# Optimization experiments

Measured on AMD Instinct MI355X. Metric: run time of the kernel, lower is better.

## Reference

```python
import jax, jax.numpy as jnp
import numpy as np

N, D, K, P = 4096, 256, 16, 3
MAXDEG = K + 1          # self loop guarantees deg >= 1, randint caps deg <= K+1
TAU, LAM, BETA, MARGIN = 0.8, 0.5, 1.0, 0.1
EPS_PD = 1e-6           # F.pairwise_distance eps (added to the difference)


def _make_adj(k):
    nbr = jax.random.randint(k, (N, K), 0, N)
    m = jnp.zeros((N, N), jnp.float32)
    m = m.at[jnp.arange(N)[:, None], nbr].set(1.0)
    m = m.at[jnp.arange(N), jnp.arange(N)].set(1.0)
    return m / m.sum(1, keepdims=True)  # row-normalized metapath adjacency


def setup_inputs():
    key = jax.random.key(0)
    ks = jax.random.split(key, 12)
    g = 1.414 * (2.0 / (D + D)) ** 0.5  # xavier_normal gain=1.414
    return {
        "h": jax.random.normal(ks[0], (N, D), jnp.float32),
        "mps": jnp.stack([_make_adj(ks[1 + i]) for i in range(P)]),
        "W_gcn": jax.random.normal(ks[4], (P, D, D), jnp.float32) * g,
        "b_gcn": jnp.zeros((P, D), jnp.float32),
        "prelu_a": jnp.full((P,), 0.25, jnp.float32),
        "att_fc_W": jax.random.normal(ks[5], (D, D), jnp.float32) * g,
        "att_fc_b": jnp.zeros((D,), jnp.float32),
        "att_vec": jax.random.normal(ks[6], (D,), jnp.float32) * g,
        "proj_W1": jax.random.normal(ks[7], (D, D), jnp.float32) * g,
        "proj_b1": jnp.zeros((D,), jnp.float32),
        "proj_W2": jax.random.normal(ks[8], (D, D), jnp.float32) * g,
        "proj_b2": jnp.zeros((D,), jnp.float32),
    }


def _gcn(h, adj, W, b, a):
    out = adj @ (h @ W.T) + b          # spmm(adj, fc(h)) + bias
    return jnp.where(out > 0, out, a * out)  # PReLU


def _node_loss(emb, adj):
    # vectorized form of the per-node nonzero/pairwise_distance loop
    mask = adj > 0                      # [N, N]
    deg = mask.sum(1)                   # [N], >= 1 via self loops
    # stable argsort: neighbors first (ascending index), matching torch.nonzero order
    pos_idx = jnp.argsort(~mask, axis=1)[:, :MAXDEG]
    neg_idx = jnp.argsort(mask, axis=1)[:, :MAXDEG]   # first deg non-neighbors
    anc = emb[:, None, :]               # anchor expanded over pairs
    dp = jnp.sum((anc - emb[pos_idx] + EPS_PD) ** 2, -1)  # [N, MAXDEG]
    dn = jnp.sum((anc - emb[neg_idx] + EPS_PD) ** 2, -1)
    valid = jnp.arange(MAXDEG)[None, :] < deg[:, None]
    per = jnp.maximum(dp - dn + MARGIN, 0.0) * valid
    return jnp.sum(per.sum(1) / deg.astype(emb.dtype))  # per-node mean, summed


def _proj(z, W1, b1, W2, b2):
    return jax.nn.elu(z @ W1.T + b1) @ W2.T + b2


def _contrast(z1, z2, pos, W1, b1, W2, b2):
    p1 = _proj(z1, W1, b1, W2, b2)
    p2 = _proj(z2, W1, b1, W2, b2)
    n1 = jnp.linalg.norm(p1, axis=-1, keepdims=True)
    n2 = jnp.linalg.norm(p2, axis=-1, keepdims=True)
    sim = jnp.exp((p1 @ p2.T) / (n1 * n2.T) / TAU)     # [N, N]
    m12 = sim / (sim.sum(1, keepdims=True) + 1e-8)
    m21 = sim.T / (sim.T.sum(1, keepdims=True) + 1e-8)
    l12 = -jnp.log((m12 * pos).sum(-1)).mean()
    l21 = -jnp.log((m21 * pos).sum(-1)).mean()
    return LAM * l12 + (1.0 - LAM) * l21


def reference(h, mps, W_gcn, b_gcn, prelu_a, att_fc_W, att_fc_b, att_vec,
              proj_W1, proj_b1, proj_W2, proj_b2):
    embeds = [_gcn(h, mps[i], W_gcn[i], b_gcn[i], prelu_a[i]) for i in range(P)]
    node_loss = sum(_node_loss(embeds[i], mps[i]) for i in range(P))
    # faithful to original control flow: i==0 inner loop overwrites self.loss,
    # so only the (0, P-1) pair survives from i==0
    closs = _contrast(embeds[0], embeds[P - 1], mps[0], proj_W1, proj_b1, proj_W2, proj_b2)
    for i in range(1, P - 1):
        for j in range(i + 1, P):
            closs = closs + _contrast(embeds[i], embeds[j], mps[i], proj_W1, proj_b1, proj_W2, proj_b2)
    # semantic attention over metapaths
    sp = jnp.stack([jnp.tanh(e @ att_fc_W.T + att_fc_b).mean(0) for e in embeds])  # [P, D]
    beta = jax.nn.softmax(sp @ att_vec)                                            # [P]
    z_mp = jnp.einsum('p,pnd->nd', beta, jnp.stack(embeds))
    return z_mp, node_loss + BETA * closs
```

## Files before the change

kernel.cpp:

```cpp
#include <hip/hip_runtime.h>
#include <hip/hip_bf16.h>

constexpr int N = 4096;
constexpr int D = 256;
constexpr int P = 3;
constexpr int MAXDEG = 17;
constexpr float TAU = 0.8f;
constexpr float MARGIN = 0.1f;
constexpr float EPS_PD = 1e-6f;

constexpr int LDP = 40;

constexpr int OFF_H    = 0;
constexpr int OFF_WG   = 1048576;
constexpr int OFF_ATTW = 1245184;
constexpr int OFF_W1   = 1310720;
constexpr int OFF_W2   = 1376256;
constexpr int OFF_BG   = 1441792;
constexpr int OFF_ATTB = 1442560;
constexpr int OFF_AV   = 1442816;
constexpr int OFF_PA   = 1443072;
constexpr int OFF_B1   = 1443328;
constexpr int OFF_B2   = 1443584;
constexpr int CONV_TOTAL = 1443840;

typedef __attribute__((ext_vector_type(8))) short bfrag8;
typedef __attribute__((ext_vector_type(4))) float facc4;

__device__ inline facc4 mfma16(bfrag8 a, bfrag8 b, facc4 c) {
    return __builtin_amdgcn_mfma_f32_16x16x32_bf16(a, b, c, 0, 0, 0);
}
__device__ inline float b2f(__hip_bfloat16 v) { return __bfloat162float(v); }
__device__ inline float bfbits2f(unsigned short u) {
    return __uint_as_float(((unsigned int)u) << 16);
}
__device__ inline unsigned short f2bfbits(float v) {
    __hip_bfloat16 t = __float2bfloat16(v);
    return *(unsigned short*)&t;
}
__device__ inline int get_bf(const int* __restrict__ counter) { return counter[0] > 100; }

__device__ inline float load_in(const void* p, size_t i, int bf) {
    return bf ? __bfloat162float(((const __hip_bfloat16*)p)[i])
              : ((const float*)p)[i];
}

__device__ __forceinline__ void gl_lds16(const __hip_bfloat16* g, __hip_bfloat16* l) {
    __builtin_amdgcn_global_load_lds(
        (const __attribute__((address_space(1))) unsigned int*)g,
        (__attribute__((address_space(3))) unsigned int*)l, 16, 0, 0);
}

__global__ void detect_dtype(const unsigned int* __restrict__ w, int nwords,
                             int* __restrict__ counter) {
    int stride = gridDim.x * blockDim.x;
    int c = 0;
    for (int i = blockIdx.x * blockDim.x + threadIdx.x; i < nwords; i += stride) {
        unsigned int x = w[i];
        if ((x & 0xFFFF0000u) == 0u && x != 0u) c++;
    }
    for (int s = 32; s > 0; s >>= 1) c += __shfl_down(c, s);
    if ((threadIdx.x & 63) == 0 && c > 0) atomicAdd(counter, c);
}

__global__ void convert_all(const void* h, const void* wg, const void* attw,
                            const void* w1, const void* w2, const void* bg,
                            const void* attb, const void* av, const void* pa,
                            const void* b1, const void* b2,
                            const int* __restrict__ counter,
                            __hip_bfloat16* __restrict__ dst) {
    int bf = get_bf(counter);
    const void* srcs[11] = {h, wg, attw, w1, w2, bg, attb, av, pa, b1, b2};
    const int offs[11] = {OFF_H, OFF_WG, OFF_ATTW, OFF_W1, OFF_W2, OFF_BG,
                          OFF_ATTB, OFF_AV, OFF_PA, OFF_B1, OFF_B2};
    const int lens[11] = {1048576, 196608, 65536, 65536, 65536, 768, 256, 256, 3, 256, 256};
    int stride = gridDim.x * blockDim.x;
    int t0 = blockIdx.x * blockDim.x + threadIdx.x;
    #pragma unroll
    for (int s = 0; s < 11; s++) {
        for (int i = t0; i < lens[s]; i += stride)
            dst[offs[s] + i] = __float2bfloat16(load_in(srcs[s], i, bf));
    }
}

__global__ void extract_sparse(const void* __restrict__ mps, const int* __restrict__ counter,
                               int* __restrict__ nbr_idx, float* __restrict__ nbr_val,
                               int* __restrict__ neg_idx, int* __restrict__ deg) {
    int bf = get_bf(counter);
    int row = blockIdx.x;
    int t = threadIdx.x;
    __shared__ int cnt;
    __shared__ int sidx[32];
    __shared__ float sval[32];
    if (t == 0) cnt = 0;
    __syncthreads();
    int e0 = t * 16;
    if (bf) {
        const uint4* base = (const uint4*)((const __hip_bfloat16*)mps + (size_t)row * N + e0);
        #pragma unroll
        for (int v = 0; v < 2; v++) {
            uint4 w = base[v];
            unsigned int ws[4] = {w.x, w.y, w.z, w.w};
            #pragma unroll
            for (int j = 0; j < 4; j++) {
                unsigned short lo = (unsigned short)(ws[j] & 0xFFFFu);
                unsigned short hi = (unsigned short)(ws[j] >> 16);
                if (lo) { int k = atomicAdd(&cnt, 1); if (k < 32) { sidx[k] = e0 + v * 8 + j * 2;     sval[k] = bfbits2f(lo); } }
                if (hi) { int k = atomicAdd(&cnt, 1); if (k < 32) { sidx[k] = e0 + v * 8 + j * 2 + 1; sval[k] = bfbits2f(hi); } }
            }
        }
    } else {
        const float4* base = (const float4*)((const float*)mps + (size_t)row * N + e0);
        #pragma unroll
        for (int v = 0; v < 4; v++) {
            float4 w = base[v];
            float ws[4] = {w.x, w.y, w.z, w.w};
            #pragma unroll
            for (int j = 0; j < 4; j++)
                if (ws[j] > 0.f) { int k = atomicAdd(&cnt, 1); if (k < 32) { sidx[k] = e0 + v * 4 + j; sval[k] = ws[j]; } }
        }
    }
    __syncthreads();
    if (t == 0) {
        int dg = cnt; if (dg > MAXDEG) dg = MAXDEG;
        for (int i = 1; i < dg; i++) {
            int ki = sidx[i]; float kv = sval[i]; int j = i - 1;
            while (j >= 0 && sidx[j] > ki) { sidx[j+1] = sidx[j]; sval[j+1] = sval[j]; j--; }
            sidx[j+1] = ki; sval[j+1] = kv;
        }
        deg[row] = dg;
        int* oi = nbr_idx + (size_t)row * MAXDEG;
        float* ov = nbr_val + (size_t)row * MAXDEG;
        int* ng = neg_idx + (size_t)row * MAXDEG;
        for (int i = 0; i < MAXDEG; i++) { oi[i] = (i < dg) ? sidx[i] : 0; ov[i] = (i < dg) ? sval[i] : 0.f; }
        int c = 0, j = 0, found = 0;
        while (found < MAXDEG) {
            if (j < dg && sidx[j] == c) { j++; c++; continue; }
            ng[found++] = c++;
        }
    }
}

template <int ACT>
__global__ void gemm_mfma(const __hip_bfloat16* __restrict__ Abase, size_t strideA,
                          const __hip_bfloat16* __restrict__ Bbase, size_t strideB,
                          const __hip_bfloat16* __restrict__ bias, size_t strideBias,
                          __hip_bfloat16* __restrict__ Cbase, size_t strideC) {
    int z = blockIdx.z;
    const __hip_bfloat16* A = Abase + (size_t)z * strideA;
    const __hip_bfloat16* B = Bbase + (size_t)z * strideB;
    __shared__ __align__(16) __hip_bfloat16 As[64 * LDP];
    __shared__ __align__(16) __hip_bfloat16 Bs[64 * LDP];
    int bm = blockIdx.x * 64, bn = blockIdx.y * 64;
    int tid = threadIdx.x, wave = tid >> 6, lane = tid & 63;
    int quad = lane >> 4, l15 = lane & 15;
    int wr = (wave & 1) * 32, wc = (wave >> 1) * 32;
    facc4 acc[2][2] = {};
    int sr = tid >> 2, kq = (tid & 3) * 8;
    for (int k0 = 0; k0 < D; k0 += 32) {
        *(bfrag8*)&As[sr * LDP + kq] = *(const bfrag8*)&A[(size_t)(bm + sr) * D + k0 + kq];
        *(bfrag8*)&Bs[sr * LDP + kq] = *(const bfrag8*)&B[(size_t)(bn + sr) * D + k0 + kq];
        __syncthreads();
        bfrag8 af[2], bfr[2];
        #pragma unroll
        for (int mi = 0; mi < 2; mi++)
            af[mi] = *(const bfrag8*)&As[(wr + mi * 16 + l15) * LDP + quad * 8];
        #pragma unroll
        for (int ni = 0; ni < 2; ni++)
            bfr[ni] = *(const bfrag8*)&Bs[(wc + ni * 16 + l15) * LDP + quad * 8];
        #pragma unroll
        for (int mi = 0; mi < 2; mi++)
            #pragma unroll
            for (int ni = 0; ni < 2; ni++)
                acc[mi][ni] = mfma16(af[mi], bfr[ni], acc[mi][ni]);
        __syncthreads();
    }
    #pragma unroll
    for (int mi = 0; mi < 2; mi++) {
        #pragma unroll
        for (int ni = 0; ni < 2; ni++) {
            int col = bn + wc + ni * 16 + l15;
            #pragma unroll
            for (int r = 0; r < 4; r++) {
                int row = bm + wr + mi * 16 + quad * 4 + r;
                float v = acc[mi][ni][r];
                if (bias) v += b2f(bias[col]);
                if (ACT == 1) v = v > 0.f ? v : expm1f(v);
                Cbase[(size_t)z * strideC + (size_t)row * D + col] = __float2bfloat16(v);
            }
        }
    }
}

__global__ void gemm_dual(const __hip_bfloat16* __restrict__ embBase,
                          const __hip_bfloat16* __restrict__ conv,
                          __hip_bfloat16* __restrict__ xbuf,
                          float* __restrict__ spacc) {
    int z = blockIdx.z;
    const __hip_bfloat16* A = embBase + (size_t)z * N * D;
    const __hip_bfloat16* Ba = conv + OFF_ATTW;
    const __hip_bfloat16* Bw = conv + OFF_W1;
    __shared__ __align__(16) __hip_bfloat16 As[64 * LDP];
    __shared__ __align__(16) __hip_bfloat16 Bsa[64 * LDP];
    __shared__ __align__(16) __hip_bfloat16 Bsw[64 * LDP];
    int bm = blockIdx.x * 64, bn = blockIdx.y * 64;
    int tid = threadIdx.x, wave = tid >> 6, lane = tid & 63;
    int quad = lane >> 4, l15 = lane & 15;
    int wr = (wave & 1) * 32, wc = (wave >> 1) * 32;
    facc4 accA[2][2] = {};
    facc4 accW[2][2] = {};
    int sr = tid >> 2, kq = (tid & 3) * 8;
    for (int k0 = 0; k0 < D; k0 += 32) {
        *(bfrag8*)&As[sr * LDP + kq]  = *(const bfrag8*)&A[(size_t)(bm + sr) * D + k0 + kq];
        *(bfrag8*)&Bsa[sr * LDP + kq] = *(const bfrag8*)&Ba[(size_t)(bn + sr) * D + k0 + kq];
        *(bfrag8*)&Bsw[sr * LDP + kq] = *(const bfrag8*)&Bw[(size_t)(bn + sr) * D + k0 + kq];
        __syncthreads();
        bfrag8 af[2], ba[2], bw[2];
        #pragma unroll
        for (int mi = 0; mi < 2; mi++)
            af[mi] = *(const bfrag8*)&As[(wr + mi * 16 + l15) * LDP + quad * 8];
        #pragma unroll
        for (int ni = 0; ni < 2; ni++) {
            ba[ni] = *(const bfrag8*)&Bsa[(wc + ni * 16 + l15) * LDP + quad * 8];
            bw[ni] = *(const bfrag8*)&Bsw[(wc + ni * 16 + l15) * LDP + quad * 8];
        }
        #pragma unroll
        for (int mi = 0; mi < 2; mi++)
            #pragma unroll
            for (int ni = 0; ni < 2; ni++) {
                accA[mi][ni] = mfma16(af[mi], ba[ni], accA[mi][ni]);
                accW[mi][ni] = mfma16(af[mi], bw[ni], accW[mi][ni]);
            }
        __syncthreads();
    }
    float cs[2] = {0.f, 0.f};
    #pragma unroll
    for (int mi = 0; mi < 2; mi++) {
        #pragma unroll
        for (int ni = 0; ni < 2; ni++) {
            int col = bn + wc + ni * 16 + l15;
            float battb = b2f(conv[OFF_ATTB + col]);
            float bb1   = b2f(conv[OFF_B1 + col]);
            #pragma unroll
            for (int r = 0; r < 4; r++) {
                int row = bm + wr + mi * 16 + quad * 4 + r;
                cs[ni] += tanhf(accA[mi][ni][r] + battb);
                float v = accW[mi][ni][r] + bb1;
                v = v > 0.f ? v : expm1f(v);
                xbuf[(size_t)z * N * D + (size_t)row * D + col] = __float2bfloat16(v);
            }
        }
    }
    #pragma unroll
    for (int ni = 0; ni < 2; ni++) {
        float v = cs[ni];
        v += __shfl_xor(v, 16); v += __shfl_xor(v, 32);
        if (quad == 0) {
            int col = bn + wc + ni * 16 + l15;
            atomicAdd(&spacc[(size_t)z * D + col], v);
        }
    }
}

__global__ void gemm_w2_norm(const __hip_bfloat16* __restrict__ xbase,
                             const __hip_bfloat16* __restrict__ conv,
                             __hip_bfloat16* __restrict__ qbase) {
    int z = blockIdx.z;
    const __hip_bfloat16* A = xbase + (size_t)z * N * D;
    const __hip_bfloat16* B = conv + OFF_W2;
    __shared__ __align__(16) __hip_bfloat16 As[16 * LDP];
    __shared__ __align__(16) __hip_bfloat16 Bs[256 * LDP];
    __shared__ float sred[4][16];
    int bm = blockIdx.x * 16;
    int tid = threadIdx.x, wave = tid >> 6, lane = tid & 63;
    int quad = lane >> 4, l15 = lane & 15;
    int wc = wave * 64;
    facc4 acc[4] = {};
    for (int k0 = 0; k0 < D; k0 += 32) {
        if (tid < 64) {
            int r = tid >> 2, kq = (tid & 3) * 8;
            *(bfrag8*)&As[r * LDP + kq] = *(const bfrag8*)&A[(size_t)(bm + r) * D + k0 + kq];
        }
        #pragma unroll
        for (int i = 0; i < 4; i++) {
            int f = tid + 256 * i;
            int r = f >> 2, kq = (f & 3) * 8;
            *(bfrag8*)&Bs[r * LDP + kq] = *(const bfrag8*)&B[(size_t)r * D + k0 + kq];
        }
        __syncthreads();
        bfrag8 af = *(const bfrag8*)&As[l15 * LDP + quad * 8];
        #pragma unroll
        for (int ni = 0; ni < 4; ni++) {
            bfrag8 bf = *(const bfrag8*)&Bs[(wc + ni * 16 + l15) * LDP + quad * 8];
            acc[ni] = mfma16(af, bf, acc[ni]);
        }
        __syncthreads();
    }
    float vv[4][4];
    #pragma unroll
    for (int ni = 0; ni < 4; ni++) {
        float bb = b2f(conv[OFF_B2 + wc + ni * 16 + l15]);
        #pragma unroll
        for (int r = 0; r < 4; r++) vv[ni][r] = acc[ni][r] + bb;
    }
    #pragma unroll
    for (int r = 0; r < 4; r++) {
        float ss = vv[0][r] * vv[0][r] + vv[1][r] * vv[1][r] +
                   vv[2][r] * vv[2][r] + vv[3][r] * vv[3][r];
        ss += __shfl_xor(ss, 1); ss += __shfl_xor(ss, 2);
        ss += __shfl_xor(ss, 4); ss += __shfl_xor(ss, 8);
        if (l15 == 0) sred[wave][quad * 4 + r] = ss;
    }
    __syncthreads();
    #pragma unroll
    for (int r = 0; r < 4; r++) {
        int rl = quad * 4 + r;
        float ssum = sred[0][rl] + sred[1][rl] + sred[2][rl] + sred[3][rl];
        float inv = rsqrtf(ssum + 1e-30f);
        int row = bm + rl;
        #pragma unroll
        for (int ni = 0; ni < 4; ni++)
            qbase[(size_t)z * N * D + (size_t)row * D + wc + ni * 16 + l15] =
                __float2bfloat16(vv[ni][r] * inv);
    }
}

__global__ void spmm_prelu(const __hip_bfloat16* __restrict__ Xbase,
                           const int* __restrict__ nbr_idx, const float* __restrict__ nbr_val,
                           const int* __restrict__ deg, const __hip_bfloat16* __restrict__ conv,
                           __hip_bfloat16* __restrict__ embBase) {
    int z = blockIdx.z;
    int wave = threadIdx.x >> 6, lane = threadIdx.x & 63;
    int n = blockIdx.x * 4 + wave;
    const __hip_bfloat16* X = Xbase + (size_t)z * N * D;
    const int* idx = nbr_idx + ((size_t)z * N + n) * MAXDEG;
    const float* val = nbr_val + ((size_t)z * N + n) * MAXDEG;
    int dg = deg[z * N + n];
    float acc[4] = {0.f, 0.f, 0.f, 0.f};
    for (int k = 0; k < dg; k++) {
        int j = idx[k];
        float vk = val[k];
        ushort4 x = *(const ushort4*)&X[(size_t)j * D + lane * 4];
        acc[0] += vk * bfbits2f(x.x); acc[1] += vk * bfbits2f(x.y);
        acc[2] += vk * bfbits2f(x.z); acc[3] += vk * bfbits2f(x.w);
    }
    ushort4 bb = *(const ushort4*)&conv[OFF_BG + z * D + lane * 4];
    float b[4] = {bfbits2f(bb.x), bfbits2f(bb.y), bfbits2f(bb.z), bfbits2f(bb.w)};
    float a = b2f(conv[OFF_PA + z]);
    ushort4 o;
    float v0 = acc[0] + b[0]; o.x = f2bfbits(v0 > 0.f ? v0 : a * v0);
    float v1 = acc[1] + b[1]; o.y = f2bfbits(v1 > 0.f ? v1 : a * v1);
    float v2 = acc[2] + b[2]; o.z = f2bfbits(v2 > 0.f ? v2 : a * v2);
    float v3 = acc[3] + b[3]; o.w = f2bfbits(v3 > 0.f ? v3 : a * v3);
    *(ushort4*)&embBase[(size_t)z * N * D + (size_t)n * D + lane * 4] = o;
}

__global__ void sim_mfma(const __hip_bfloat16* __restrict__ q,
                         float* __restrict__ rowsum, float* __restrict__ colsum) {
    int pair = blockIdx.z;
    const __hip_bfloat16* Qa = q + (size_t)pair * N * D;
    const __hip_bfloat16* Qb = q + (size_t)2 * N * D;
    __shared__ __align__(16) __hip_bfloat16 As[128 * 64];
    __shared__ __align__(16) __hip_bfloat16 Bs[128 * 64];
    int bm = blockIdx.x * 128, bn = blockIdx.y * 128;
    int tid = threadIdx.x, wave = tid >> 6, lane = tid & 63;
    int quad = lane >> 4, l15 = lane & 15;
    int wr = (wave & 1) * 64, wc = (wave >> 1) * 64;
    facc4 acc[4][4] = {};
    int sr0 = tid >> 3;
    int cc  = tid & 7;
    for (int k0 = 0; k0 < D; k0 += 64) {
        #pragma unroll
        for (int i = 0; i < 4; i++) {
            int r = sr0 + 32 * i;
            int cg = (cc ^ (r & 7)) * 8;
            gl_lds16(&Qa[(size_t)(bm + r) * D + k0 + cg], &As[r * 64 + cc * 8]);
            gl_lds16(&Qb[(size_t)(bn + r) * D + k0 + cg], &Bs[r * 64 + cc * 8]);
        }
        __syncthreads();
        #pragma unroll
        for (int kk = 0; kk < 64; kk += 32) {
            int kb = kk >> 3;
            bfrag8 af[4], bfr[4];
            #pragma unroll
            for (int mi = 0; mi < 4; mi++) {
                int R = wr + mi * 16 + l15;
                int pc = ((kb + quad) ^ (l15 & 7)) * 8;
                af[mi] = *(const bfrag8*)&As[R * 64 + pc];
            }
            #pragma unroll
            for (int ni = 0; ni < 4; ni++) {
                int R = wc + ni * 16 + l15;
                int pc = ((kb + quad) ^ (l15 & 7)) * 8;
                bfr[ni] = *(const bfrag8*)&Bs[R * 64 + pc];
            }
            #pragma unroll
            for (int mi = 0; mi < 4; mi++)
                #pragma unroll
                for (int ni = 0; ni < 4; ni++)
                    acc[mi][ni] = mfma16(af[mi], bfr[ni], acc[mi][ni]);
        }
        __syncthreads();
    }
    constexpr float invtau = 1.0f / TAU;
    float rs[4][4];
    float cs[4] = {0.f, 0.f, 0.f, 0.f};
    #pragma unroll
    for (int mi = 0; mi < 4; mi++)
        #pragma unroll
        for (int r = 0; r < 4; r++) rs[mi][r] = 0.f;
    #pragma unroll
    for (int mi = 0; mi < 4; mi++)
        #pragma unroll
        for (int ni = 0; ni < 4; ni++)
            #pragma unroll
            for (int r = 0; r < 4; r++) {
                float e = __expf(acc[mi][ni][r] * invtau);
                rs[mi][r] += e;
                cs[ni] += e;
            }
    #pragma unroll
    for (int mi = 0; mi < 4; mi++)
        #pragma unroll
        for (int r = 0; r < 4; r++) {
            float v = rs[mi][r];
            v += __shfl_xor(v, 1); v += __shfl_xor(v, 2);
            v += __shfl_xor(v, 4); v += __shfl_xor(v, 8);
            rs[mi][r] = v;
        }
    if (l15 == 0) {
        #pragma unroll
        for (int mi = 0; mi < 4; mi++)
            #pragma unroll
            for (int r = 0; r < 4; r++)
                atomicAdd(&rowsum[(size_t)pair * N + bm + wr + mi * 16 + quad * 4 + r], rs[mi][r]);
    }
    #pragma unroll
    for (int ni = 0; ni < 4; ni++) {
        float v = cs[ni];
        v += __shfl_xor(v, 16); v += __shfl_xor(v, 32);
        if (quad == 0)
            atomicAdd(&colsum[(size_t)pair * N + bn + wc + ni * 16 + l15], v);
    }
}

__global__ void edge_losses(const __hip_bfloat16* __restrict__ embBase,
                            const __hip_bfloat16* __restrict__ q,
                            const int* __restrict__ nbr_idx, const float* __restrict__ nbr_val,
                            const int* __restrict__ neg_idx, const int* __restrict__ deg,
                            float* __restrict__ nlpart,
                            float* __restrict__ pdrow, float* __restrict__ pdcol) {
    int z = blockIdx.z;
    int wave = threadIdx.x >> 6, lane = threadIdx.x & 63;
    int n = blockIdx.x * 4 + wave;
    if (z < P) {
        const __hip_bfloat16* emb = embBase + (size_t)z * N * D;
        int dg = deg[z * N + n];
        const int* ip = nbr_idx + ((size_t)z * N + n) * MAXDEG;
        const int* ig = neg_idx + ((size_t)z * N + n) * MAXDEG;
        ushort4 ar = *(const ushort4*)&emb[(size_t)n * D + lane * 4];
        float a[4] = {bfbits2f(ar.x), bfbits2f(ar.y), bfbits2f(ar.z), bfbits2f(ar.w)};
        float s = 0.f;
        for (int k = 0; k < dg; k++) {
            int jp = ip[k], jn = ig[k];
            ushort4 pr = *(const ushort4*)&emb[(size_t)jp * D + lane * 4];
            ushort4 nr = *(const ushort4*)&emb[(size_t)jn * D + lane * 4];
            float dp = 0.f, dn = 0.f;
            float x0 = a[0] - bfbits2f(pr.x) + EPS_PD, y0 = a[0] - bfbits2f(nr.x) + EPS_PD;
            float x1 = a[1] - bfbits2f(pr.y) + EPS_PD, y1 = a[1] - bfbits2f(nr.y) + EPS_PD;
            float x2 = a[2] - bfbits2f(pr.z) + EPS_PD, y2 = a[2] - bfbits2f(nr.z) + EPS_PD;
            float x3 = a[3] - bfbits2f(pr.w) + EPS_PD, y3 = a[3] - bfbits2f(nr.w) + EPS_PD;
            dp = x0 * x0 + x1 * x1 + x2 * x2 + x3 * x3;
            dn = y0 * y0 + y1 * y1 + y2 * y2 + y3 * y3;
            #pragma unroll
            for (int st = 1; st <= 32; st <<= 1) { dp += __shfl_xor(dp, st); dn += __shfl_xor(dn, st); }
            float v = dp - dn + MARGIN;
            s += v > 0.f ? v : 0.f;
        }
        if (lane == 0) nlpart[z * N + n] = s / (float)dg;
    } else {
        int pair = z - P;
        const __hip_bfloat16* Qa = q + (size_t)pair * N * D;
        const __hip_bfloat16* Qb = q + (size_t)2 * N * D;
        int dg = deg[pair * N + n];
        const int* idx = nbr_idx + ((size_t)pair * N + n) * MAXDEG;
        const float* val = nbr_val + ((size_t)pair * N + n) * MAXDEG;
        const float invtau = 1.0f / TAU;
        ushort4 ar = *(const ushort4*)&Qa[(size_t)n * D + lane * 4];
        ushort4 br = *(const ushort4*)&Qb[(size_t)n * D + lane * 4];
        float a[4] = {bfbits2f(ar.x), bfbits2f(ar.y), bfbits2f(ar.z), bfbits2f(ar.w)};
        float b[4] = {bfbits2f(br.x), bfbits2f(br.y), bfbits2f(br.z), bfbits2f(br.w)};
        float sr = 0.f, sc = 0.f;
        for (int k = 0; k < dg; k++) {
            int j = idx[k];
            ushort4 pj = *(const ushort4*)&Qb[(size_t)j * D + lane * 4];
            ushort4 aj = *(const ushort4*)&Qa[(size_t)j * D + lane * 4];
            float dr = a[0] * bfbits2f(pj.x) + a[1] * bfbits2f(pj.y) +
                       a[2] * bfbits2f(pj.z) + a[3] * bfbits2f(pj.w);
            float dc = b[0] * bfbits2f(aj.x) + b[1] * bfbits2f(aj.y) +
                       b[2] * bfbits2f(aj.z) + b[3] * bfbits2f(aj.w);
            #pragma unroll
            for (int s = 1; s <= 32; s <<= 1) { dr += __shfl_xor(dr, s); dc += __shfl_xor(dc, s); }
            sr += __expf(dr * invtau) * val[k];
            sc += __expf(dc * invtau) * val[k];
        }
        if (lane == 0) { pdrow[pair * N + n] = sr; pdcol[pair * N + n] = sc; }
    }
}

__global__ void reduce_loss_beta(const float* __restrict__ nlpart,
                                 const float* __restrict__ rowsum, const float* __restrict__ colsum,
                                 const float* __restrict__ pdrow, const float* __restrict__ pdcol,
                                 const float* __restrict__ spacc,
                                 const __hip_bfloat16* __restrict__ conv,
                                 float* __restrict__ beta, float* __restrict__ loss) {
    int t = threadIdx.x;
    __shared__ float red[256];
    __shared__ float w[P];
    for (int p = 0; p < P; p++) {
        float v = (spacc[p * D + t] / (float)N) * b2f(conv[OFF_AV + t]);
        red[t] = v;
        __syncthreads();
        for (int s = 128; s > 0; s >>= 1) { if (t < s) red[t] += red[t + s]; __syncthreads(); }
        if (t == 0) w[p] = red[0];
        __syncthreads();
    }
    float s = 0.f;
    for (int i = t; i < P * N; i += 256) s += nlpart[i];
    for (int i = t; i < 2 * N; i += 256) {
        float l12 = -logf(pdrow[i] / (rowsum[i] + 1e-8f));
        float l21 = -logf(pdcol[i] / (colsum[i] + 1e-8f));
        s += (0.5f * l12 + 0.5f * l21) / (float)N;
    }
    red[t] = s;
    __syncthreads();
    for (int st = 128; st > 0; st >>= 1) { if (t < st) red[t] += red[t + st]; __syncthreads(); }
    if (t == 0) {
        loss[0] = red[0];
        float m = fmaxf(w[0], fmaxf(w[1], w[2]));
        float e0 = __expf(w[0] - m), e1 = __expf(w[1] - m), e2 = __expf(w[2] - m);
        float ssum = e0 + e1 + e2;
        beta[0] = e0 / ssum; beta[1] = e1 / ssum; beta[2] = e2 / ssum;
    }
}

__global__ void zmp_out(const __hip_bfloat16* __restrict__ embBase, const float* __restrict__ beta,
                        const float* __restrict__ loss, const int* __restrict__ counter,
                        void* __restrict__ out) {
    int bf = get_bf(counter);
    int i = blockIdx.x * 256 + threadIdx.x;
    float v = beta[0] * b2f(embBase[i]) + beta[1] * b2f(embBase[(size_t)N * D + i]) +
              beta[2] * b2f(embBase[(size_t)2 * N * D + i]);
    if (bf) {
        __hip_bfloat16* o = (__hip_bfloat16*)out;
        o[i] = __float2bfloat16(v);
        if (i == 0) o[(size_t)N * D] = __float2bfloat16(*loss);
    } else {
        float* o = (float*)out;
        o[i] = v;
        if (i == 0) o[(size_t)N * D] = *loss;
    }
}

extern "C" void kernel_launch(void* const* d_in, const int* in_sizes, int n_in,
                              void* d_out, int out_size, void* d_ws, size_t ws_size,
                              hipStream_t stream) {
    const void* h        = d_in[0];
    const void* mps      = d_in[1];
    const void* W_gcn    = d_in[2];
    const void* b_gcn    = d_in[3];
    const void* prelu_a  = d_in[4];
    const void* att_fc_W = d_in[5];
    const void* att_fc_b = d_in[6];
    const void* att_vec  = d_in[7];
    const void* proj_W1  = d_in[8];
    const void* proj_b1  = d_in[9];
    const void* proj_W2  = d_in[10];
    const void* proj_b2  = d_in[11];

    char* ws = (char*)d_ws;
    size_t off = 0;
    auto alloc = [&](size_t bytes) -> char* {
        char* p = ws + off;
        off = (off + bytes + 255) & ~(size_t)255;
        return p;
    };
    __hip_bfloat16* conv = (__hip_bfloat16*)alloc((size_t)CONV_TOTAL * 2);
    __hip_bfloat16* xbuf = (__hip_bfloat16*)alloc((size_t)P * N * D * 2);
    __hip_bfloat16* emb  = (__hip_bfloat16*)alloc((size_t)P * N * D * 2);
    __hip_bfloat16* q    = (__hip_bfloat16*)alloc((size_t)P * N * D * 2);
    int*   nbr_idx = (int*)alloc((size_t)P * N * MAXDEG * 4);
    float* nbr_val = (float*)alloc((size_t)P * N * MAXDEG * 4);
    int*   neg_idx = (int*)alloc((size_t)P * N * MAXDEG * 4);
    int*   deg     = (int*)alloc((size_t)P * N * 4);
    float* nlpart  = (float*)alloc((size_t)P * N * 4);
    float* pdrow   = (float*)alloc((size_t)2 * N * 4);
    float* pdcol   = (float*)alloc((size_t)2 * N * 4);
    char* zero_begin = ws + off;
    float* rowsum = (float*)alloc((size_t)2 * N * 4);
    float* colsum = (float*)alloc((size_t)2 * N * 4);
    float* spacc  = (float*)alloc((size_t)P * D * 4);
    float* beta   = (float*)alloc(16);
    float* loss   = (float*)alloc(16);
    int*   counter = (int*)alloc(16);
    size_t zero_bytes = (size_t)((ws + off) - zero_begin);
    hipMemsetAsync(zero_begin, 0, zero_bytes, stream);

    detect_dtype<<<1024, 256, 0, stream>>>((const unsigned int*)mps, 2 * 1024 * 1024, counter);

    convert_all<<<512, 256, 0, stream>>>(h, W_gcn, att_fc_W, proj_W1, proj_W2, b_gcn,
                                         att_fc_b, att_vec, prelu_a, proj_b1, proj_b2,
                                         counter, conv);

    extract_sparse<<<P * N, 256, 0, stream>>>(mps, counter, nbr_idx, nbr_val, neg_idx, deg);

    dim3 ggrid(N / 64, D / 64, P);
    size_t nd = (size_t)N * D;
    gemm_mfma<0><<<ggrid, 256, 0, stream>>>(
        conv + OFF_H, 0, conv + OFF_WG, (size_t)D * D, nullptr, 0, xbuf, nd);
    spmm_prelu<<<dim3(N / 4, 1, P), 256, 0, stream>>>(xbuf, nbr_idx, nbr_val, deg, conv, emb);
    gemm_dual<<<ggrid, 256, 0, stream>>>(emb, conv, xbuf, spacc);
    gemm_w2_norm<<<dim3(N / 16, 1, P), 256, 0, stream>>>(xbuf, conv, q);
    sim_mfma<<<dim3(N / 128, N / 128, 2), 256, 0, stream>>>(q, rowsum, colsum);
    edge_losses<<<dim3(N / 4, 1, P + 2), 256, 0, stream>>>(emb, q, nbr_idx, nbr_val,
                                                           neg_idx, deg, nlpart, pdrow, pdcol);
    reduce_loss_beta<<<1, 256, 0, stream>>>(nlpart, rowsum, colsum, pdrow, pdcol,
                                            spacc, conv, beta, loss);
    zmp_out<<<(N * D) / 256, 256, 0, stream>>>(emb, beta, loss, counter, d_out);
}
```

Before: 499.3 us.

## Parallelize sparse row sort, fuse three GCN GEMMs, shuffle-broadcast neighbor lists

Several independent changes. The single-thread insertion sort and negative-index scan in extract_sparse become a 64-thread rank sort plus a ballot-based scan. The three per-metapath X=hW^T GEMMs are merged into one kernel that reuses the loaded h tile across all three weight matrices. spmm_prelu and edge_losses load the neighbor index and value lists once per wave and broadcast them with shuffles, and spmm is unrolled by two. zmp_out is vectorized to four elements per thread. Together these aim to cut serial work per row, redundant loads of h and neighbor lists, and launch count, at the cost of higher register and LDS use in the fused GEMM.

New measurement: 476.2 us. 1.05x faster.

```diff
diff --git a/kernel.cpp b/kernel.cpp
--- a/kernel.cpp
+++ b/kernel.cpp
@@ -121,75 +121,80 @@
         }
     }
     __syncthreads();
-    if (t == 0) {
+    if (t < 64) {
         int dg = cnt; if (dg > MAXDEG) dg = MAXDEG;
-        for (int i = 1; i < dg; i++) {
-            int ki = sidx[i]; float kv = sval[i]; int j = i - 1;
-            while (j >= 0 && sidx[j] > ki) { sidx[j+1] = sidx[j]; sval[j+1] = sval[j]; j--; }
-            sidx[j+1] = ki; sval[j+1] = kv;
-        }
-        deg[row] = dg;
-        int* oi = nbr_idx + (size_t)row * MAXDEG;
-        float* ov = nbr_val + (size_t)row * MAXDEG;
-        int* ng = neg_idx + (size_t)row * MAXDEG;
-        for (int i = 0; i < MAXDEG; i++) { oi[i] = (i < dg) ? sidx[i] : 0; ov[i] = (i < dg) ? sval[i] : 0.f; }
-        int c = 0, j = 0, found = 0;
-        while (found < MAXDEG) {
-            if (j < dg && sidx[j] == c) { j++; c++; continue; }
-            ng[found++] = c++;
-        }
-    }
-}
-
-template <int ACT>
-__global__ void gemm_mfma(const __hip_bfloat16* __restrict__ Abase, size_t strideA,
-                          const __hip_bfloat16* __restrict__ Bbase, size_t strideB,
-                          const __hip_bfloat16* __restrict__ bias, size_t strideBias,
-                          __hip_bfloat16* __restrict__ Cbase, size_t strideC) {
-    int z = blockIdx.z;
-    const __hip_bfloat16* A = Abase + (size_t)z * strideA;
-    const __hip_bfloat16* B = Bbase + (size_t)z * strideB;
+        int myidx = 0; float myval = 0.f; int rank = 0;
+        if (t < dg) {
+            myidx = sidx[t]; myval = sval[t];
+            for (int j = 0; j < dg; j++) rank += (sidx[j] < myidx) ? 1 : 0;
+        }
+        if (t < dg) { sidx[rank] = myidx; sval[rank] = myval; }
+        if (t < MAXDEG) {
+            nbr_idx[(size_t)row * MAXDEG + t] = (t < dg) ? sidx[t] : 0;
+            nbr_val[(size_t)row * MAXDEG + t] = (t < dg) ? sval[t] : 0.f;
+        }
+        if (t == 0) deg[row] = dg;
+        int c = t;
+        bool cand = (c < dg + MAXDEG);
+        bool isnbr = false;
+        if (cand) for (int j = 0; j < dg; j++) isnbr |= (sidx[j] == c);
+        bool nonnbr = cand && !isnbr;
+        unsigned long long m = __ballot(nonnbr);
+        int nrank = __popcll(m & ((c < 64) ? ((1ull << c) - 1ull) : ~0ull));
+        if (nonnbr && nrank < MAXDEG) neg_idx[(size_t)row * MAXDEG + nrank] = c;
+    }
+}
+
+__global__ void gemm_triple(const __hip_bfloat16* __restrict__ conv,
+                            __hip_bfloat16* __restrict__ xbuf) {
+    const __hip_bfloat16* A = conv + OFF_H;
     __shared__ __align__(16) __hip_bfloat16 As[64 * LDP];
-    __shared__ __align__(16) __hip_bfloat16 Bs[64 * LDP];
+    __shared__ __align__(16) __hip_bfloat16 Bs[3][64 * LDP];
     int bm = blockIdx.x * 64, bn = blockIdx.y * 64;
     int tid = threadIdx.x, wave = tid >> 6, lane = tid & 63;
     int quad = lane >> 4, l15 = lane & 15;
     int wr = (wave & 1) * 32, wc = (wave >> 1) * 32;
-    facc4 acc[2][2] = {};
+    facc4 acc[3][2][2] = {};
     int sr = tid >> 2, kq = (tid & 3) * 8;
     for (int k0 = 0; k0 < D; k0 += 32) {
         *(bfrag8*)&As[sr * LDP + kq] = *(const bfrag8*)&A[(size_t)(bm + sr) * D + k0 + kq];
-        *(bfrag8*)&Bs[sr * LDP + kq] = *(const bfrag8*)&B[(size_t)(bn + sr) * D + k0 + kq];
-        __syncthreads();
-        bfrag8 af[2], bfr[2];
+        #pragma unroll
+        for (int z = 0; z < 3; z++)
+            *(bfrag8*)&Bs[z][sr * LDP + kq] =
+                *(const bfrag8*)&conv[OFF_WG + (size_t)z * D * D + (size_t)(bn + sr) * D + k0 + kq];
+        __syncthreads();
+        bfrag8 af[2];
         #pragma unroll
         for (int mi = 0; mi < 2; mi++)
             af[mi] = *(const bfrag8*)&As[(wr + mi * 16 + l15) * LDP + quad * 8];
         #pragma unroll
-        for (int ni = 0; ni < 2; ni++)
-            bfr[ni] = *(const bfrag8*)&Bs[(wc + ni * 16 + l15) * LDP + quad * 8];
+        for (int z = 0; z < 3; z++) {
+            bfrag8 bfr[2];
+            #pragma unroll
+            for (int ni = 0; ni < 2; ni++)
+                bfr[ni] = *(const bfrag8*)&Bs[z][(wc + ni * 16 + l15) * LDP + quad * 8];
+            #pragma unroll
+            for (int mi = 0; mi < 2; mi++)
+                #pragma unroll
+                for (int ni = 0; ni < 2; ni++)
+                    acc[z][mi][ni] = mfma16(af[mi], bfr[ni], acc[z][mi][ni]);
+        }
+        __syncthreads();
+    }
+    #pragma unroll
+    for (int z = 0; z < 3; z++)
         #pragma unroll
         for (int mi = 0; mi < 2; mi++)
             #pragma unroll
-            for (int ni = 0; ni < 2; ni++)
-                acc[mi][ni] = mfma16(af[mi], bfr[ni], acc[mi][ni]);
-        __syncthreads();
-    }
-    #pragma unroll
-    for (int mi = 0; mi < 2; mi++) {
-        #pragma unroll
-        for (int ni = 0; ni < 2; ni++) {
-            int col = bn + wc + ni * 16 + l15;
-            #pragma unroll
-            for (int r = 0; r < 4; r++) {
-                int row = bm + wr + mi * 16 + quad * 4 + r;
-                float v = acc[mi][ni][r];
-                if (bias) v += b2f(bias[col]);
-                if (ACT == 1) v = v > 0.f ? v : expm1f(v);
-                Cbase[(size_t)z * strideC + (size_t)row * D + col] = __float2bfloat16(v);
+            for (int ni = 0; ni < 2; ni++) {
+                int col = bn + wc + ni * 16 + l15;
+                #pragma unroll
+                for (int r = 0; r < 4; r++) {
+                    int row = bm + wr + mi * 16 + quad * 4 + r;
+                    xbuf[(size_t)z * N * D + (size_t)row * D + col] =
+                        __float2bfloat16(acc[z][mi][ni][r]);
+                }
             }
-        }
-    }
 }
 
 __global__ void gemm_dual(const __hip_bfloat16* __restrict__ embBase,
@@ -333,25 +338,37 @@
     int wave = threadIdx.x >> 6, lane = threadIdx.x & 63;
     int n = blockIdx.x * 4 + wave;
     const __hip_bfloat16* X = Xbase + (size_t)z * N * D;
-    const int* idx = nbr_idx + ((size_t)z * N + n) * MAXDEG;
-    const float* val = nbr_val + ((size_t)z * N + n) * MAXDEG;
     int dg = deg[z * N + n];
+    int idxv = 0; float valv = 0.f;
+    if (lane < MAXDEG) {
+        idxv = nbr_idx[((size_t)z * N + n) * MAXDEG + lane];
+        valv = nbr_val[((size_t)z * N + n) * MAXDEG + lane];
+    }
     float acc[4] = {0.f, 0.f, 0.f, 0.f};
-    for (int k = 0; k < dg; k++) {
-        int j = idx[k];
-        float vk = val[k];
-        ushort4 x = *(const ushort4*)&X[(size_t)j * D + lane * 4];
-        acc[0] += vk * bfbits2f(x.x); acc[1] += vk * bfbits2f(x.y);
-        acc[2] += vk * bfbits2f(x.z); acc[3] += vk * bfbits2f(x.w);
+    int k = 0;
+    for (; k + 1 < dg; k += 2) {
+        int j0 = __shfl(idxv, k), j1 = __shfl(idxv, k + 1);
+        float v0 = __shfl(valv, k), v1 = __shfl(valv, k + 1);
+        ushort4 x0 = *(const ushort4*)&X[(size_t)j0 * D + lane * 4];
+        ushort4 x1 = *(const ushort4*)&X[(size_t)j1 * D + lane * 4];
+        acc[0] += v0 * bfbits2f(x0.x) + v1 * bfbits2f(x1.x);
+        acc[1] += v0 * bfbits2f(x0.y) + v1 * bfbits2f(x1.y);
+        acc[2] += v0 * bfbits2f(x0.z) + v1 * bfbits2f(x1.z);
+        acc[3] += v0 * bfbits2f(x0.w) + v1 * bfbits2f(x1.w);
+    }
+    if (k < dg) {
+        int j0 = __shfl(idxv, k); float v0 = __shfl(valv, k);
+        ushort4 x0 = *(const ushort4*)&X[(size_t)j0 * D + lane * 4];
+        acc[0] += v0 * bfbits2f(x0.x); acc[1] += v0 * bfbits2f(x0.y);
+        acc[2] += v0 * bfbits2f(x0.z); acc[3] += v0 * bfbits2f(x0.w);
     }
     ushort4 bb = *(const ushort4*)&conv[OFF_BG + z * D + lane * 4];
-    float b[4] = {bfbits2f(bb.x), bfbits2f(bb.y), bfbits2f(bb.z), bfbits2f(bb.w)};
     float a = b2f(conv[OFF_PA + z]);
     ushort4 o;
-    float v0 = acc[0] + b[0]; o.x = f2bfbits(v0 > 0.f ? v0 : a * v0);
-    float v1 = acc[1] + b[1]; o.y = f2bfbits(v1 > 0.f ? v1 : a * v1);
-    float v2 = acc[2] + b[2]; o.z = f2bfbits(v2 > 0.f ? v2 : a * v2);
-    float v3 = acc[3] + b[3]; o.w = f2bfbits(v3 > 0.f ? v3 : a * v3);
+    float v0 = acc[0] + bfbits2f(bb.x); o.x = f2bfbits(v0 > 0.f ? v0 : a * v0);
+    float v1 = acc[1] + bfbits2f(bb.y); o.y = f2bfbits(v1 > 0.f ? v1 : a * v1);
+    float v2 = acc[2] + bfbits2f(bb.z); o.z = f2bfbits(v2 > 0.f ? v2 : a * v2);
+    float v3 = acc[3] + bfbits2f(bb.w); o.w = f2bfbits(v3 > 0.f ? v3 : a * v3);
     *(ushort4*)&embBase[(size_t)z * N * D + (size_t)n * D + lane * 4] = o;
 }
 
@@ -456,22 +473,24 @@
     if (z < P) {
         const __hip_bfloat16* emb = embBase + (size_t)z * N * D;
         int dg = deg[z * N + n];
-        const int* ip = nbr_idx + ((size_t)z * N + n) * MAXDEG;
-        const int* ig = neg_idx + ((size_t)z * N + n) * MAXDEG;
+        int ipv = 0, igv = 0;
+        if (lane < MAXDEG) {
+            ipv = nbr_idx[((size_t)z * N + n) * MAXDEG + lane];
+            igv = neg_idx[((size_t)z * N + n) * MAXDEG + lane];
+        }
         ushort4 ar = *(const ushort4*)&emb[(size_t)n * D + lane * 4];
         float a[4] = {bfbits2f(ar.x), bfbits2f(ar.y), bfbits2f(ar.z), bfbits2f(ar.w)};
         float s = 0.f;
         for (int k = 0; k < dg; k++) {
-            int jp = ip[k], jn = ig[k];
+            int jp = __shfl(ipv, k), jn = __shfl(igv, k);
             ushort4 pr = *(const ushort4*)&emb[(size_t)jp * D + lane * 4];
             ushort4 nr = *(const ushort4*)&emb[(size_t)jn * D + lane * 4];
-            float dp = 0.f, dn = 0.f;
             float x0 = a[0] - bfbits2f(pr.x) + EPS_PD, y0 = a[0] - bfbits2f(nr.x) + EPS_PD;
             float x1 = a[1] - bfbits2f(pr.y) + EPS_PD, y1 = a[1] - bfbits2f(nr.y) + EPS_PD;
             float x2 = a[2] - bfbits2f(pr.z) + EPS_PD, y2 = a[2] - bfbits2f(nr.z) + EPS_PD;
             float x3 = a[3] - bfbits2f(pr.w) + EPS_PD, y3 = a[3] - bfbits2f(nr.w) + EPS_PD;
-            dp = x0 * x0 + x1 * x1 + x2 * x2 + x3 * x3;
-            dn = y0 * y0 + y1 * y1 + y2 * y2 + y3 * y3;
+            float dp = x0 * x0 + x1 * x1 + x2 * x2 + x3 * x3;
+            float dn = y0 * y0 + y1 * y1 + y2 * y2 + y3 * y3;
             #pragma unroll
             for (int st = 1; st <= 32; st <<= 1) { dp += __shfl_xor(dp, st); dn += __shfl_xor(dn, st); }
             float v = dp - dn + MARGIN;
@@ -483,8 +502,11 @@
         const __hip_bfloat16* Qa = q + (size_t)pair * N * D;
         const __hip_bfloat16* Qb = q + (size_t)2 * N * D;
         int dg = deg[pair * N + n];
-        const int* idx = nbr_idx + ((size_t)pair * N + n) * MAXDEG;
-        const float* val = nbr_val + ((size_t)pair * N + n) * MAXDEG;
+        int idxv = 0; float valv = 0.f;
+        if (lane < MAXDEG) {
+            idxv = nbr_idx[((size_t)pair * N + n) * MAXDEG + lane];
+            valv = nbr_val[((size_t)pair * N + n) * MAXDEG + lane];
+        }
         const float invtau = 1.0f / TAU;
         ushort4 ar = *(const ushort4*)&Qa[(size_t)n * D + lane * 4];
         ushort4 br = *(const ushort4*)&Qb[(size_t)n * D + lane * 4];
@@ -492,7 +514,8 @@
         float b[4] = {bfbits2f(br.x), bfbits2f(br.y), bfbits2f(br.z), bfbits2f(br.w)};
         float sr = 0.f, sc = 0.f;
         for (int k = 0; k < dg; k++) {
-            int j = idx[k];
+            int j = __shfl(idxv, k);
+            float vk = __shfl(valv, k);
             ushort4 pj = *(const ushort4*)&Qb[(size_t)j * D + lane * 4];
             ushort4 aj = *(const ushort4*)&Qa[(size_t)j * D + lane * 4];
             float dr = a[0] * bfbits2f(pj.x) + a[1] * bfbits2f(pj.y) +
@@ -500,9 +523,9 @@
             float dc = b[0] * bfbits2f(aj.x) + b[1] * bfbits2f(aj.y) +
                        b[2] * bfbits2f(aj.z) + b[3] * bfbits2f(aj.w);
             #pragma unroll
-            for (int s = 1; s <= 32; s <<= 1) { dr += __shfl_xor(dr, s); dc += __shfl_xor(dc, s); }
-            sr += __expf(dr * invtau) * val[k];
-            sc += __expf(dc * invtau) * val[k];
+            for (int s2 = 1; s2 <= 32; s2 <<= 1) { dr += __shfl_xor(dr, s2); dc += __shfl_xor(dc, s2); }
+            sr += __expf(dr * invtau) * vk;
+            sc += __expf(dc * invtau) * vk;
         }
         if (lane == 0) { pdrow[pair * N + n] = sr; pdcol[pair * N + n] = sc; }
     }
@@ -548,16 +571,26 @@
                         const float* __restrict__ loss, const int* __restrict__ counter,
                         void* __restrict__ out) {
     int bf = get_bf(counter);
-    int i = blockIdx.x * 256 + threadIdx.x;
-    float v = beta[0] * b2f(embBase[i]) + beta[1] * b2f(embBase[(size_t)N * D + i]) +
-              beta[2] * b2f(embBase[(size_t)2 * N * D + i]);
+    int i = (blockIdx.x * 256 + threadIdx.x) * 4;
+    ushort4 e0 = *(const ushort4*)&embBase[i];
+    ushort4 e1 = *(const ushort4*)&embBase[(size_t)N * D + i];
+    ushort4 e2 = *(const ushort4*)&embBase[(size_t)2 * N * D + i];
+    float b0 = beta[0], b1 = beta[1], b2 = beta[2];
+    float v[4];
+    v[0] = b0 * bfbits2f(e0.x) + b1 * bfbits2f(e1.x) + b2 * bfbits2f(e2.x);
+    v[1] = b0 * bfbits2f(e0.y) + b1 * bfbits2f(e1.y) + b2 * bfbits2f(e2.y);
+    v[2] = b0 * bfbits2f(e0.z) + b1 * bfbits2f(e1.z) + b2 * bfbits2f(e2.z);
+    v[3] = b0 * bfbits2f(e0.w) + b1 * bfbits2f(e1.w) + b2 * bfbits2f(e2.w);
     if (bf) {
         __hip_bfloat16* o = (__hip_bfloat16*)out;
-        o[i] = __float2bfloat16(v);
+        ushort4 ov;
+        ov.x = f2bfbits(v[0]); ov.y = f2bfbits(v[1]);
+        ov.z = f2bfbits(v[2]); ov.w = f2bfbits(v[3]);
+        *(ushort4*)&o[i] = ov;
         if (i == 0) o[(size_t)N * D] = __float2bfloat16(*loss);
     } else {
         float* o = (float*)out;
-        o[i] = v;
+        o[i] = v[0]; o[i + 1] = v[1]; o[i + 2] = v[2]; o[i + 3] = v[3];
         if (i == 0) o[(size_t)N * D] = *loss;
     }
 }
@@ -614,17 +647,15 @@
 
     extract_sparse<<<P * N, 256, 0, stream>>>(mps, counter, nbr_idx, nbr_val, neg_idx, deg);
 
-    dim3 ggrid(N / 64, D / 64, P);
     size_t nd = (size_t)N * D;
-    gemm_mfma<0><<<ggrid, 256, 0, stream>>>(
-        conv + OFF_H, 0, conv + OFF_WG, (size_t)D * D, nullptr, 0, xbuf, nd);
+    gemm_triple<<<dim3(N / 64, D / 64), 256, 0, stream>>>(conv, xbuf);
     spmm_prelu<<<dim3(N / 4, 1, P), 256, 0, stream>>>(xbuf, nbr_idx, nbr_val, deg, conv, emb);
-    gemm_dual<<<ggrid, 256, 0, stream>>>(emb, conv, xbuf, spacc);
+    gemm_dual<<<dim3(N / 64, D / 64, P), 256, 0, stream>>>(emb, conv, xbuf, spacc);
     gemm_w2_norm<<<dim3(N / 16, 1, P), 256, 0, stream>>>(xbuf, conv, q);
     sim_mfma<<<dim3(N / 128, N / 128, 2), 256, 0, stream>>>(q, rowsum, colsum);
     edge_losses<<<dim3(N / 4, 1, P + 2), 256, 0, stream>>>(emb, q, nbr_idx, nbr_val,
                                                            neg_idx, deg, nlpart, pdrow, pdcol);
     reduce_loss_beta<<<1, 256, 0, stream>>>(nlpart, rowsum, colsum, pdrow, pdcol,
                                             spacc, conv, beta, loss);
-    zmp_out<<<(N * D) / 256, 256, 0, stream>>>(emb, beta, loss, counter, d_out);
-}
+    zmp_out<<<(N * D) / 1024, 256, 0, stream>>>(emb, beta, loss, counter, d_out);
+}
```
